# Kernel optimization log

Hardware: AMD Instinct MI355X
Metric: run time of the kernel (lower is better)

The kernel has to match this reference:

```python
import jax, jax.numpy as jnp
import numpy as np


def setup_inputs() -> dict:
    key = jax.random.key(0)
    inputs = jax.random.normal(key, (8, 2048, 512), dtype=jnp.float32)
    return {"inputs": inputs}


def reference(inputs) -> jnp.ndarray:
    # score[b,i,j] = <x_i, x_j>  (no 1/sqrt(d) scaling in the original)
    score = jnp.einsum("bsd,btd->bst", inputs, inputs)  # [B,S,S]
    distribution = jax.nn.softmax(score, axis=-1)
    # output = distribution @ inputs
    return jnp.einsum("bst,btd->bsd", distribution, inputs)
```

## Files before the change

kernel.cpp:

```cpp
#include <hip/hip_runtime.h>
#include <hip/hip_bf16.h>

#define BATCH 8
#define SEQ   2048
#define DIM   512
#define QB    64
#define KB    64
#define NT    512
#define NKV   (SEQ / KB)

typedef __attribute__((ext_vector_type(8))) short short8;
typedef __attribute__((ext_vector_type(4))) float f32x4;
typedef __attribute__((ext_vector_type(4))) unsigned short ushort4v;

__device__ __forceinline__ unsigned short f2bf(float f) {
    union { float f; unsigned u; } v; v.f = f;
    return (unsigned short)((v.u + 0x7FFFu + ((v.u >> 16) & 1u)) >> 16);
}

__global__ __launch_bounds__(NT, 2)
void attn_fwd(const float* __restrict__ X, float* __restrict__ O) {
    const int b   = blockIdx.x & 7;
    const int qt  = blockIdx.x >> 3;
    const int tid = threadIdx.x;
    const int lane = tid & 63;
    const int w    = tid >> 6;
    const int col  = lane & 15;
    const int kgrp = lane >> 4;

    __shared__ unsigned short Klds[KB * DIM];
    __shared__ float Sbuf[QB][KB + 4];
    __shared__ unsigned short Plds[QB * KB];
    __shared__ float m_s[QB], l_s[QB], fac_s[QB];

    const float* Xb = X + (size_t)b * SEQ * DIM;

    const int qs  = w >> 1;
    const int kc0 = (w & 1) * 2;
    short8 qfrag[16];
    {
        const int qrow = qt * QB + qs * 16 + col;
        const float* qp = Xb + (size_t)qrow * DIM;
        #pragma unroll
        for (int ks = 0; ks < 16; ++ks) {
            const int d0 = ks * 32 + kgrp * 8;
            float4 a = *(const float4*)(qp + d0);
            float4 c = *(const float4*)(qp + d0 + 4);
            short8 q8;
            q8[0] = f2bf(a.x); q8[1] = f2bf(a.y); q8[2] = f2bf(a.z); q8[3] = f2bf(a.w);
            q8[4] = f2bf(c.x); q8[5] = f2bf(c.y); q8[6] = f2bf(c.z); q8[7] = f2bf(c.w);
            qfrag[ks] = q8;
        }
    }

    if (tid < QB) { m_s[tid] = -INFINITY; l_s[tid] = 0.f; }

    f32x4 oacc[4][4];
    #pragma unroll
    for (int i = 0; i < 4; ++i)
        #pragma unroll
        for (int j = 0; j < 4; ++j)
            oacc[i][j] = (f32x4){0.f, 0.f, 0.f, 0.f};

    for (int t = 0; t < NKV; ++t) {
        __syncthreads();
        {
            const float* kp = Xb + (size_t)(t * KB) * DIM;
            #pragma unroll
            for (int it = 0; it < 16; ++it) {
                const int idx = it * NT + tid;
                const int kv  = idx >> 7;
                const int d0  = (idx & 127) * 4;
                float4 v = *(const float4*)(kp + kv * DIM + d0);
                ushort4v h;
                h[0] = f2bf(v.x); h[1] = f2bf(v.y); h[2] = f2bf(v.z); h[3] = f2bf(v.w);
                *(ushort4v*)&Klds[kv * DIM + (d0 ^ ((kv & 7) << 3))] = h;
            }
        }
        __syncthreads();

        #pragma unroll
        for (int i = 0; i < 2; ++i) {
            const int kc = kc0 + i;
            const int kvrow = kc * 16 + col;
            const unsigned short* kbase = &Klds[kvrow * DIM];
            const int sw = (kvrow & 7) << 3;
            f32x4 sacc = (f32x4){0.f, 0.f, 0.f, 0.f};
            #pragma unroll
            for (int ks = 0; ks < 16; ++ks) {
                const int d0 = (ks * 32 + kgrp * 8) ^ sw;
                short8 kfr = *(const short8*)(kbase + d0);
                sacc = __builtin_amdgcn_mfma_f32_16x16x32_bf16(qfrag[ks], kfr, sacc, 0, 0, 0);
            }
            #pragma unroll
            for (int r = 0; r < 4; ++r)
                Sbuf[qs * 16 + kgrp * 4 + r][kc * 16 + col] = sacc[r];
        }
        __syncthreads();

        {
            const int r   = tid >> 3;
            const int sub = tid & 7;
            float4 sa = *(const float4*)&Sbuf[r][sub * 8];
            float4 sb = *(const float4*)&Sbuf[r][sub * 8 + 4];
            float mloc = fmaxf(fmaxf(fmaxf(sa.x, sa.y), fmaxf(sa.z, sa.w)),
                               fmaxf(fmaxf(sb.x, sb.y), fmaxf(sb.z, sb.w)));
            mloc = fmaxf(mloc, __shfl_xor(mloc, 1));
            mloc = fmaxf(mloc, __shfl_xor(mloc, 2));
            mloc = fmaxf(mloc, __shfl_xor(mloc, 4));
            const float mold = m_s[r];
            const float mnew = fmaxf(mold, mloc);
            const float fac  = __expf(mold - mnew);
            float p0 = __expf(sa.x - mnew), p1 = __expf(sa.y - mnew);
            float p2 = __expf(sa.z - mnew), p3 = __expf(sa.w - mnew);
            float p4 = __expf(sb.x - mnew), p5 = __expf(sb.y - mnew);
            float p6 = __expf(sb.z - mnew), p7 = __expf(sb.w - mnew);
            float lsum = ((p0 + p1) + (p2 + p3)) + ((p4 + p5) + (p6 + p7));
            lsum += __shfl_xor(lsum, 1);
            lsum += __shfl_xor(lsum, 2);
            lsum += __shfl_xor(lsum, 4);
            short8 p8;
            p8[0] = f2bf(p0); p8[1] = f2bf(p1); p8[2] = f2bf(p2); p8[3] = f2bf(p3);
            p8[4] = f2bf(p4); p8[5] = f2bf(p5); p8[6] = f2bf(p6); p8[7] = f2bf(p7);
            *(short8*)&Plds[r * KB + ((sub * 8) ^ ((r & 7) << 3))] = p8;
            if (sub == 0) {
                m_s[r] = mnew;
                fac_s[r] = fac;
                l_s[r] = l_s[r] * fac + lsum;
            }
        }
        __syncthreads();

        #pragma unroll
        for (int q2 = 0; q2 < 4; ++q2) {
            #pragma unroll
            for (int r = 0; r < 4; ++r) {
                const float f = fac_s[q2 * 16 + kgrp * 4 + r];
                #pragma unroll
                for (int dt = 0; dt < 4; ++dt) oacc[q2][dt][r] *= f;
            }
        }
        #pragma unroll
        for (int kc2 = 0; kc2 < 2; ++kc2) {
            const int kvb = kc2 * 32 + kgrp * 8;
            short8 bfr[4];
            #pragma unroll
            for (int dt = 0; dt < 4; ++dt) {
                const int d = w * 64 + dt * 16 + col;
                short8 bv;
                #pragma unroll
                for (int j = 0; j < 8; ++j) {
                    const int kv = kvb + j;
                    bv[j] = (short)Klds[kv * DIM + (d ^ ((kv & 7) << 3))];
                }
                bfr[dt] = bv;
            }
            #pragma unroll
            for (int q2 = 0; q2 < 4; ++q2) {
                const int q = q2 * 16 + col;
                short8 pfr = *(const short8*)&Plds[q * KB + (kvb ^ ((q & 7) << 3))];
                #pragma unroll
                for (int dt = 0; dt < 4; ++dt)
                    oacc[q2][dt] = __builtin_amdgcn_mfma_f32_16x16x32_bf16(pfr, bfr[dt], oacc[q2][dt], 0, 0, 0);
            }
        }
    }

    #pragma unroll
    for (int q2 = 0; q2 < 4; ++q2) {
        #pragma unroll
        for (int r = 0; r < 4; ++r) {
            const int row = q2 * 16 + kgrp * 4 + r;
            const float inv = 1.f / l_s[row];
            float* op = O + ((size_t)b * SEQ + qt * QB + row) * DIM + w * 64 + col;
            #pragma unroll
            for (int dt = 0; dt < 4; ++dt)
                op[dt * 16] = oacc[q2][dt][r] * inv;
        }
    }
}

extern "C" void kernel_launch(void* const* d_in, const int* in_sizes, int n_in,
                              void* d_out, int out_size, void* d_ws, size_t ws_size,
                              hipStream_t stream) {
    const float* X = (const float*)d_in[0];
    float* Out = (float*)d_out;
    dim3 grid(BATCH * (SEQ / QB));
    dim3 block(NT);
    hipLaunchKernelGGL(attn_fwd, grid, block, 0, stream, X, Out);
}
```

Measured before the change: 206.3 us.

## Reuse K fragments across two query tiles and swizzle LDS for PV reads

Each warp now computes QK scores for two 16-row query sub-tiles sharing each K fragment read. This halves LDS K reads per MFMA in the score phase at the cost of holding twice the Q fragments in registers. The K LDS swizzle gains extra XOR terms to reduce bank conflicts on the column-wise PV B-fragment gathers. P is stored in a fragment-ordered layout so each lane does one contiguous vector read, and the K-load loop is only partially unrolled to limit register pressure.

```diff
diff --git a/kernel.cpp b/kernel.cpp
--- a/kernel.cpp
+++ b/kernel.cpp
@@ -18,6 +18,10 @@
     return (unsigned short)((v.u + 0x7FFFu + ((v.u >> 16) & 1u)) >> 16);
 }
 
+__device__ __forceinline__ int swz(int kv) {
+    return (8 * (kv & 7)) ^ (16 * ((kv >> 3) & 3)) ^ (64 * ((kv >> 3) & 1));
+}
+
 __global__ __launch_bounds__(NT, 2)
 void attn_fwd(const float* __restrict__ X, float* __restrict__ O) {
     const int b   = blockIdx.x & 7;
@@ -28,18 +32,19 @@
     const int col  = lane & 15;
     const int kgrp = lane >> 4;
 
-    __shared__ unsigned short Klds[KB * DIM];
-    __shared__ float Sbuf[QB][KB + 4];
-    __shared__ unsigned short Plds[QB * KB];
+    __shared__ alignas(16) unsigned short Klds[KB * DIM];
+    __shared__ alignas(16) float Sbuf[QB][KB + 4];
+    __shared__ alignas(16) unsigned short Pfrag[4][2][64][8];
     __shared__ float m_s[QB], l_s[QB], fac_s[QB];
 
     const float* Xb = X + (size_t)b * SEQ * DIM;
 
-    const int qs  = w >> 1;
-    const int kc0 = (w & 1) * 2;
-    short8 qfrag[16];
-    {
-        const int qrow = qt * QB + qs * 16 + col;
+    const int qh = w >> 2;
+    const int kc = w & 3;
+    short8 qfrag[2][16];
+    #pragma unroll
+    for (int qq = 0; qq < 2; ++qq) {
+        const int qrow = qt * QB + qh * 32 + qq * 16 + col;
         const float* qp = Xb + (size_t)qrow * DIM;
         #pragma unroll
         for (int ks = 0; ks < 16; ++ks) {
@@ -49,7 +54,7 @@
             short8 q8;
             q8[0] = f2bf(a.x); q8[1] = f2bf(a.y); q8[2] = f2bf(a.z); q8[3] = f2bf(a.w);
             q8[4] = f2bf(c.x); q8[5] = f2bf(c.y); q8[6] = f2bf(c.z); q8[7] = f2bf(c.w);
-            qfrag[ks] = q8;
+            qfrag[qq][ks] = q8;
         }
     }
 
@@ -66,43 +71,44 @@
         __syncthreads();
         {
             const float* kp = Xb + (size_t)(t * KB) * DIM;
-            #pragma unroll
+            #pragma unroll 4
             for (int it = 0; it < 16; ++it) {
                 const int idx = it * NT + tid;
                 const int kv  = idx >> 7;
                 const int d0  = (idx & 127) * 4;
-                float4 v = *(const float4*)(kp + kv * DIM + d0);
+                float4 v = *(const float4*)(kp + (size_t)kv * DIM + d0);
                 ushort4v h;
                 h[0] = f2bf(v.x); h[1] = f2bf(v.y); h[2] = f2bf(v.z); h[3] = f2bf(v.w);
-                *(ushort4v*)&Klds[kv * DIM + (d0 ^ ((kv & 7) << 3))] = h;
+                *(ushort4v*)&Klds[kv * DIM + (d0 ^ swz(kv))] = h;
             }
         }
         __syncthreads();
 
-        #pragma unroll
-        for (int i = 0; i < 2; ++i) {
-            const int kc = kc0 + i;
+        {
             const int kvrow = kc * 16 + col;
             const unsigned short* kbase = &Klds[kvrow * DIM];
-            const int sw = (kvrow & 7) << 3;
-            f32x4 sacc = (f32x4){0.f, 0.f, 0.f, 0.f};
+            const int sw = swz(kvrow);
+            f32x4 sacc0 = (f32x4){0.f,0.f,0.f,0.f};
+            f32x4 sacc1 = (f32x4){0.f,0.f,0.f,0.f};
             #pragma unroll
             for (int ks = 0; ks < 16; ++ks) {
-                const int d0 = (ks * 32 + kgrp * 8) ^ sw;
-                short8 kfr = *(const short8*)(kbase + d0);
-                sacc = __builtin_amdgcn_mfma_f32_16x16x32_bf16(qfrag[ks], kfr, sacc, 0, 0, 0);
+                short8 kfr = *(const short8*)(kbase + ((ks * 32 + kgrp * 8) ^ sw));
+                sacc0 = __builtin_amdgcn_mfma_f32_16x16x32_bf16(qfrag[0][ks], kfr, sacc0, 0, 0, 0);
+                sacc1 = __builtin_amdgcn_mfma_f32_16x16x32_bf16(qfrag[1][ks], kfr, sacc1, 0, 0, 0);
             }
             #pragma unroll
-            for (int r = 0; r < 4; ++r)
-                Sbuf[qs * 16 + kgrp * 4 + r][kc * 16 + col] = sacc[r];
+            for (int r = 0; r < 4; ++r) {
+                Sbuf[qh * 32 + 0  + kgrp * 4 + r][kc * 16 + col] = sacc0[r];
+                Sbuf[qh * 32 + 16 + kgrp * 4 + r][kc * 16 + col] = sacc1[r];
+            }
         }
         __syncthreads();
 
         {
-            const int r   = tid >> 3;
-            const int sub = tid & 7;
-            float4 sa = *(const float4*)&Sbuf[r][sub * 8];
-            float4 sb = *(const float4*)&Sbuf[r][sub * 8 + 4];
+            const int r = tid >> 3;
+            const int c = tid & 7;
+            float4 sa = *(const float4*)&Sbuf[r][c * 8];
+            float4 sb = *(const float4*)&Sbuf[r][c * 8 + 4];
             float mloc = fmaxf(fmaxf(fmaxf(sa.x, sa.y), fmaxf(sa.z, sa.w)),
                                fmaxf(fmaxf(sb.x, sb.y), fmaxf(sb.z, sb.w)));
             mloc = fmaxf(mloc, __shfl_xor(mloc, 1));
@@ -122,8 +128,8 @@
             short8 p8;
             p8[0] = f2bf(p0); p8[1] = f2bf(p1); p8[2] = f2bf(p2); p8[3] = f2bf(p3);
             p8[4] = f2bf(p4); p8[5] = f2bf(p5); p8[6] = f2bf(p6); p8[7] = f2bf(p7);
-            *(short8*)&Plds[r * KB + ((sub * 8) ^ ((r & 7) << 3))] = p8;
-            if (sub == 0) {
+            *(short8*)&Pfrag[r >> 4][c >> 2][(r & 15) + 16 * (c & 3)][0] = p8;
+            if (c == 0) {
                 m_s[r] = mnew;
                 fac_s[r] = fac;
                 l_s[r] = l_s[r] * fac + lsum;
@@ -143,6 +149,10 @@
         #pragma unroll
         for (int kc2 = 0; kc2 < 2; ++kc2) {
             const int kvb = kc2 * 32 + kgrp * 8;
+            short8 afr[4];
+            #pragma unroll
+            for (int q2 = 0; q2 < 4; ++q2)
+                afr[q2] = *(const short8*)&Pfrag[q2][kc2][lane][0];
             short8 bfr[4];
             #pragma unroll
             for (int dt = 0; dt < 4; ++dt) {
@@ -151,18 +161,15 @@
                 #pragma unroll
                 for (int j = 0; j < 8; ++j) {
                     const int kv = kvb + j;
-                    bv[j] = (short)Klds[kv * DIM + (d ^ ((kv & 7) << 3))];
+                    bv[j] = (short)Klds[kv * DIM + (d ^ swz(kv))];
                 }
                 bfr[dt] = bv;
             }
             #pragma unroll
-            for (int q2 = 0; q2 < 4; ++q2) {
-                const int q = q2 * 16 + col;
-                short8 pfr = *(const short8*)&Plds[q * KB + (kvb ^ ((q & 7) << 3))];
+            for (int dt = 0; dt < 4; ++dt)
                 #pragma unroll
-                for (int dt = 0; dt < 4; ++dt)
-                    oacc[q2][dt] = __builtin_amdgcn_mfma_f32_16x16x32_bf16(pfr, bfr[dt], oacc[q2][dt], 0, 0, 0);
-            }
+                for (int q2 = 0; q2 < 4; ++q2)
+                    oacc[q2][dt] = __builtin_amdgcn_mfma_f32_16x16x32_bf16(afr[q2], bfr[dt], oacc[q2][dt], 0, 0, 0);
         }
     }
 
```

Result: slower. 458.0 us (+122.1%).
